# Kernel optimization log

Hardware: AMD Instinct MI355X
Metric: run time of the kernel (lower is better)

Reference implementation:

```python
import jax, jax.numpy as jnp
import numpy as np

COUPLING = 1.0
DT = 1.0
ATTR = 1.0
AFF_SCALE = 0.25          # feedback_affinity_scale
ALPHA_FAC = 0.25 * 1.0    # feedback_alpha_scale * alpha_scale (eval mode)
CHUNK = 256               # coupling_chunk_size
C_IN = 3                  # input_channels


def _pairwise_coupling(theta, spikes):
    """All-pairs vector Kuramoto coupling within one channel group.
    theta: [B, n, D], spikes: [B, n] -> [B, n, D]
    Chunked over receiver nodes i (lax.scan) to avoid [B,n,n,D] materialization."""
    B, n, D = theta.shape
    rng = jnp.clip(spikes.max(axis=1, keepdims=True) - spikes.min(axis=1, keepdims=True), 1e-6)  # [B,1]
    nchunks = n // CHUNK
    theta_i = theta.reshape(B, nchunks, CHUNK, D).transpose(1, 0, 2, 3)   # [nc,B,C,D]
    spike_i = spikes.reshape(B, nchunks, CHUNK).transpose(1, 0, 2)        # [nc,B,C]

    def body(_, xs):
        ti, si = xs                                              # [B,C,D], [B,C]
        nd = jnp.abs(si[:, :, None] - spikes[:, None, :]) / rng[:, :, None]   # [B,C,n]
        aff = AFF_SCALE * (1.0 - nd)
        alpha = ALPHA_FAC * nd
        # sin(theta_j - theta_i - alpha_ij): [B,C,n,D]
        phase = jnp.sin(theta[:, None, :, :] - ti[:, :, None, :] - alpha[..., None])
        out = (COUPLING / n) * jnp.sum(aff[..., None] * phase, axis=2)        # [B,C,D]
        return None, out

    _, outs = jax.lax.scan(body, None, (theta_i, spike_i))       # [nc,B,C,D]
    return outs.transpose(1, 0, 2, 3).reshape(B, n, D)


def _channel_wise_coupling(theta, spikes):
    """HWC flatten: channel c occupies nodes c, c+C, c+2C, ..."""
    B, N, D = theta.shape
    nc = N // C_IN
    th = theta.reshape(B, nc, C_IN, D).transpose(2, 0, 1, 3)     # [C_IN,B,nc,D]
    sp = spikes.reshape(B, nc, C_IN).transpose(2, 0, 1)          # [C_IN,B,nc]
    outs = jax.vmap(_pairwise_coupling)(th, sp)                  # [C_IN,B,nc,D]
    return outs.transpose(1, 2, 0, 3).reshape(B, N, D)


def setup_inputs() -> dict:
    key = jax.random.key(0)
    k1, k2, k3 = jax.random.split(key, 3)
    B, N, D = 4, 12288, 4
    return {
        "theta_prev": jax.random.normal(k1, (B, N, D), dtype=jnp.float32),
        "gamma_prev": jax.random.normal(k2, (B, N, D), dtype=jnp.float32),
        "affinity": jax.random.uniform(k3, (B, N), dtype=jnp.float32),
    }


def reference(theta_prev, gamma_prev, affinity):
    coupling_term = _channel_wise_coupling(theta_prev, affinity)
    theta_dot = ATTR * (gamma_prev - theta_prev) + coupling_term
    theta_next = theta_prev + DT * theta_dot
    # torch.nn.functional.normalize: x / max(||x||_2, eps)
    norm = jnp.maximum(jnp.linalg.norm(theta_next, axis=-1, keepdims=True), 1e-6)
    return theta_next / norm
```

## Files before the change

kernel.cpp:

```cpp
#include <hip/hip_runtime.h>
#include <math.h>

#define BATCH 4
#define NN    12288
#define CIN   3
#define NC    4096
#define NG    12
#define NB    128
#define HS3   3
#define PSZ   (4 * NB * 2)
#define HSTR  9

#define SC_OFF 0
#define P_OFF  64
#define H2_OFF (P_OFF + 192 * PSZ)

__launch_bounds__(256)
__global__ void k_hist(const float* __restrict__ spikes,
                       const float* __restrict__ theta,
                       float* __restrict__ ws) {
    __shared__ float lh[4 * NB * HS3];
    __shared__ float smn[4], smx[4];
    __shared__ float uScale, uAmin;

    int blk = blockIdx.x, g = blk >> 4, chunk = blk & 15;
    int b = g / CIN, c = g % CIN;
    int tid = threadIdx.x, lane = tid & 63, w = tid >> 6;

    #pragma unroll
    for (int q = 0; q < 6; ++q) lh[tid + q * 256] = 0.f;

    const float4* row = (const float4*)(spikes + b * NN);
    float mn = 1e30f, mx = -1e30f;
    #pragma unroll
    for (int q = 0; q < 12; ++q) {
        int f = tid + q * 256;
        float4 v4 = row[f];
        float e[4] = {v4.x, v4.y, v4.z, v4.w};
        int r  = (4 * f) % 3;
        int j0 = (c - r + 3) % 3;
        mn = fminf(mn, e[j0]); mx = fmaxf(mx, e[j0]);
        if (j0 + 3 < 4) { mn = fminf(mn, e[j0 + 3]); mx = fmaxf(mx, e[j0 + 3]); }
    }
    #pragma unroll
    for (int off = 32; off; off >>= 1) {
        mn = fminf(mn, __shfl_down(mn, off));
        mx = fmaxf(mx, __shfl_down(mx, off));
    }
    if (lane == 0) { smn[w] = mn; smx[w] = mx; }
    __syncthreads();
    if (tid == 0) {
        float m0 = fminf(fminf(smn[0], smn[1]), fminf(smn[2], smn[3]));
        float m1 = fmaxf(fmaxf(smx[0], smx[1]), fmaxf(smx[2], smx[3]));
        float scale = 0.25f / fmaxf(m1 - m0, 1e-6f);
        uScale = scale;
        uAmin  = m0 * scale;
    }
    __syncthreads();
    float scale = uScale, amin = uAmin;

    int k = chunk * 256 + tid;
    int v = b * NN + k * CIN + c;
    float a = spikes[v] * scale;
    int bb = (int)((a - amin) * (4.0f * NB));
    bb = bb < 0 ? 0 : (bb > NB - 1 ? NB - 1 : bb);
    float4 th = ((const float4*)theta)[v];
    float thv[4] = {th.x, th.y, th.z, th.w};
    #pragma unroll
    for (int d = 0; d < 4; ++d) {
        float sth, cth; __sincosf(thv[d], &sth, &cth);
        float* h = lh + (d * NB + bb) * HS3;
        atomicAdd(h + 0, sth);
        atomicAdd(h + 1, cth);
    }
    __syncthreads();

    float* P = ws + P_OFF + (size_t)blk * PSZ;
    #pragma unroll
    for (int q = 0; q < 4; ++q) {
        int o = tid + q * 256;
        P[o] = lh[(o >> 1) * HS3 + (o & 1)];
    }
    if (chunk == 0 && tid == 0) {
        ws[SC_OFF + g * 2]     = scale;
        ws[SC_OFF + g * 2 + 1] = amin;
    }
}

__launch_bounds__(256)
__global__ void k_mscan(float* __restrict__ ws) {
    __shared__ float raw[256];
    __shared__ float lh[NB * HSTR];
    int gd = blockIdx.x, g = gd >> 2, d = gd & 3;
    int tid = threadIdx.x, lane = tid & 63, w = tid >> 6;

    const float* Pg = ws + P_OFF + (size_t)(g * 16) * PSZ + d * (NB * 2);
    float s = 0.f;
    #pragma unroll
    for (int p = 0; p < 16; ++p) s += Pg[(size_t)p * PSZ + tid];
    raw[tid] = s;
    __syncthreads();

    float amin = ws[SC_OFF + g * 2 + 1];
    if (tid < NB) {
        float Ss = raw[tid * 2], Sc = raw[tid * 2 + 1];
        float abar = amin + ((float)tid + 0.5f) * (0.25f / (float)NB);
        float sa, ca; __sincosf(abar, &sa, &ca);
        float c0 = fmaf(ca, Ss,  sa * Sc);
        float c1 = fmaf(ca, Sc, -sa * Ss);
        float c4 = fmaf(ca, Ss, -sa * Sc);
        float c5 = fmaf(ca, Sc,  sa * Ss);
        float* L = lh + tid * HSTR;
        L[0] = c0;        L[1] = c1;
        L[2] = abar * c0; L[3] = abar * c1;
        L[4] = c4;        L[5] = c5;
        L[6] = abar * c4; L[7] = abar * c5;
    }
    __syncthreads();

    #pragma unroll
    for (int p = 0; p < 2; ++p) {
        int ch = w * 2 + p;
        float x0 = lh[(lane * 2 + 0) * HSTR + ch];
        float x1 = lh[(lane * 2 + 1) * HSTR + ch];
        float i0 = x0, i1 = i0 + x1;
        float incl = i1;
        #pragma unroll
        for (int off = 1; off < 64; off <<= 1) {
            float o = __shfl_up(incl, off);
            if (lane >= off) incl += o;
        }
        float ebt = incl - i1;
        lh[(lane * 2 + 0) * HSTR + ch] = ebt + i0;
        lh[(lane * 2 + 1) * HSTR + ch] = ebt + i1;
    }
    __syncthreads();

    float* H2 = ws + H2_OFF + (size_t)gd * (NB * 8);
    #pragma unroll
    for (int q = 0; q < 4; ++q) {
        int o = tid + q * 256;
        H2[o] = lh[(o >> 3) * HSTR + (o & 7)];
    }
}

__launch_bounds__(256)
__global__ void k_apply(const float* __restrict__ spikes,
                        const float* __restrict__ theta,
                        const float* __restrict__ gamma,
                        const float* __restrict__ ws,
                        float* __restrict__ out) {
    __shared__ __align__(16) float lH[CIN * 4 * NB * 8];
    int v = blockIdx.x * 256 + threadIdx.x;
    int b = v / NN;

    const float4* src = (const float4*)(ws + H2_OFF + (size_t)b * (CIN * 4 * NB * 8));
    float4* dst = (float4*)lH;
    #pragma unroll
    for (int q = 0; q < 12; ++q) {
        int i = threadIdx.x + q * 256;
        dst[i] = src[i];
    }
    __syncthreads();

    int r = v - b * NN;
    int c = r % 3;
    int g = b * CIN + c;
    float scale = ws[SC_OFF + g * 2], amin = ws[SC_OFF + g * 2 + 1];
    float a = spikes[v] * scale;
    int bb = (int)((a - amin) * (4.0f * NB));
    bb = bb < 0 ? 0 : (bb > NB - 1 ? NB - 1 : bb);
    float sa, ca; __sincosf(a, &sa, &ca);
    float4 th = ((const float4*)theta)[v];
    float4 gm = ((const float4*)gamma)[v];
    float thv[4] = {th.x, th.y, th.z, th.w};
    float cp[4];
    #pragma unroll
    for (int d = 0; d < 4; ++d) {
        float sth, cth; __sincosf(thv[d], &sth, &cth);
        float sf = fmaf(cth, sa,  sth * ca);
        float cf = fmaf(-sth, sa, cth * ca);
        float sp = fmaf(-cth, sa, sth * ca);
        float cq = fmaf(sth, sa,  cth * ca);
        const float4* Hq = (const float4*)(lH + (c * 4 + d) * (NB * 8));
        float4 Plo = Hq[bb * 2];
        float4 Phi = Hq[bb * 2 + 1];
        float4 T   = Hq[(NB - 1) * 2 + 1];
        float lowS = fmaf(0.25f - a, Plo.x, Plo.z);
        float lowC = fmaf(0.25f - a, Plo.y, Plo.w);
        float lower = cf * lowS - sf * lowC;
        float S4 = T.x - Phi.x, S5 = T.y - Phi.y;
        float S6 = T.z - Phi.z, S7 = T.w - Phi.w;
        float upS = fmaf(0.25f + a, S4, -S6);
        float upC = fmaf(0.25f + a, S5, -S7);
        float upper = cq * upS - sp * upC;
        cp[d] = (lower + upper) * (1.0f / (float)NC);
    }
    float tx = gm.x + cp[0], ty = gm.y + cp[1];
    float tz = gm.z + cp[2], tw = gm.w + cp[3];
    float nrm = sqrtf(tx * tx + ty * ty + tz * tz + tw * tw);
    float inv = 1.0f / fmaxf(nrm, 1e-6f);
    ((float4*)out)[v] = make_float4(tx * inv, ty * inv, tz * inv, tw * inv);
}

extern "C" void kernel_launch(void* const* d_in, const int* in_sizes, int n_in,
                              void* d_out, int out_size, void* d_ws, size_t ws_size,
                              hipStream_t stream) {
    const float* theta  = (const float*)d_in[0];
    const float* gamma  = (const float*)d_in[1];
    const float* spikes = (const float*)d_in[2];
    float* out = (float*)d_out;
    float* ws  = (float*)d_ws;

    hipLaunchKernelGGL(k_hist,  dim3(NG * 16),       dim3(256), 0, stream, spikes, theta, ws);
    hipLaunchKernelGGL(k_mscan, dim3(NG * 4),        dim3(256), 0, stream, ws);
    hipLaunchKernelGGL(k_apply, dim3(BATCH*NN/256),  dim3(256), 0, stream,
                       spikes, theta, gamma, ws, out);
}
```

Measured before the change: 70.89 us.

## Split stats into own kernel and parallelize hist/apply per dimension element

Moves the per-group min/max reduction into a separate k_stats kernel so k_hist no longer recomputes it in every block. k_hist now launches four times as many blocks, each thread handling one (node, dim) pair, and k_mscan reduces 64 partials instead of 16. k_apply maps one thread per output element, reads the prefix tables directly from global memory instead of staging them in LDS, and computes the norm with lane shuffles. This trades one extra launch, more partial-sum traffic and uncached table reads for more parallelism and no per-block LDS staging.

Result: slower. 75.31 us (+6.2%).

```diff
diff --git a/kernel.cpp b/kernel.cpp
--- a/kernel.cpp
+++ b/kernel.cpp
@@ -7,30 +7,17 @@
 #define NC    4096
 #define NG    12
 #define NB    128
-#define HS3   3
-#define PSZ   (4 * NB * 2)
 #define HSTR  9
 
 #define SC_OFF 0
 #define P_OFF  64
-#define H2_OFF (P_OFF + 192 * PSZ)
+#define H2_OFF (P_OFF + 768 * 1024)
 
 __launch_bounds__(256)
-__global__ void k_hist(const float* __restrict__ spikes,
-                       const float* __restrict__ theta,
-                       float* __restrict__ ws) {
-    __shared__ float lh[4 * NB * HS3];
-    __shared__ float smn[4], smx[4];
-    __shared__ float uScale, uAmin;
-
-    int blk = blockIdx.x, g = blk >> 4, chunk = blk & 15;
-    int b = g / CIN, c = g % CIN;
+__global__ void k_stats(const float* __restrict__ spikes, float* __restrict__ ws) {
+    int g = blockIdx.x, b = g / CIN, c = g % CIN;
+    const float4* row = (const float4*)(spikes + b * NN);
     int tid = threadIdx.x, lane = tid & 63, w = tid >> 6;
-
-    #pragma unroll
-    for (int q = 0; q < 6; ++q) lh[tid + q * 256] = 0.f;
-
-    const float4* row = (const float4*)(spikes + b * NN);
     float mn = 1e30f, mx = -1e30f;
     #pragma unroll
     for (int q = 0; q < 12; ++q) {
@@ -47,43 +34,48 @@
         mn = fminf(mn, __shfl_down(mn, off));
         mx = fmaxf(mx, __shfl_down(mx, off));
     }
+    __shared__ float smn[4], smx[4];
     if (lane == 0) { smn[w] = mn; smx[w] = mx; }
     __syncthreads();
     if (tid == 0) {
         float m0 = fminf(fminf(smn[0], smn[1]), fminf(smn[2], smn[3]));
         float m1 = fmaxf(fmaxf(smx[0], smx[1]), fmaxf(smx[2], smx[3]));
         float scale = 0.25f / fmaxf(m1 - m0, 1e-6f);
-        uScale = scale;
-        uAmin  = m0 * scale;
+        ws[SC_OFF + g * 2]     = scale;
+        ws[SC_OFF + g * 2 + 1] = m0 * scale;
     }
+}
+
+__launch_bounds__(256)
+__global__ void k_hist(const float* __restrict__ spikes,
+                       const float* __restrict__ theta,
+                       float* __restrict__ ws) {
+    __shared__ float lh[4 * NB * 3];
+    int blk = blockIdx.x, g = blk >> 6, j = blk & 63;
+    int b = g / CIN, c = g % CIN;
+    int tid = threadIdx.x;
+    #pragma unroll
+    for (int q = 0; q < 6; ++q) lh[tid + q * 256] = 0.f;
+    float scale = ws[SC_OFF + g * 2], amin = ws[SC_OFF + g * 2 + 1];
     __syncthreads();
-    float scale = uScale, amin = uAmin;
 
-    int k = chunk * 256 + tid;
+    int k = j * 64 + (tid >> 2);
+    int d = tid & 3;
     int v = b * NN + k * CIN + c;
     float a = spikes[v] * scale;
     int bb = (int)((a - amin) * (4.0f * NB));
     bb = bb < 0 ? 0 : (bb > NB - 1 ? NB - 1 : bb);
-    float4 th = ((const float4*)theta)[v];
-    float thv[4] = {th.x, th.y, th.z, th.w};
-    #pragma unroll
-    for (int d = 0; d < 4; ++d) {
-        float sth, cth; __sincosf(thv[d], &sth, &cth);
-        float* h = lh + (d * NB + bb) * HS3;
-        atomicAdd(h + 0, sth);
-        atomicAdd(h + 1, cth);
-    }
+    float sth, cth; __sincosf(theta[v * 4 + d], &sth, &cth);
+    float* h = lh + (d * NB + bb) * 3;
+    atomicAdd(h + 0, sth);
+    atomicAdd(h + 1, cth);
     __syncthreads();
 
-    float* P = ws + P_OFF + (size_t)blk * PSZ;
+    float* P = ws + P_OFF + (size_t)blk * 1024;
     #pragma unroll
     for (int q = 0; q < 4; ++q) {
         int o = tid + q * 256;
-        P[o] = lh[(o >> 1) * HS3 + (o & 1)];
-    }
-    if (chunk == 0 && tid == 0) {
-        ws[SC_OFF + g * 2]     = scale;
-        ws[SC_OFF + g * 2 + 1] = amin;
+        P[o] = lh[(o >> 1) * 3 + (o & 1)];
     }
 }
 
@@ -94,10 +86,10 @@
     int gd = blockIdx.x, g = gd >> 2, d = gd & 3;
     int tid = threadIdx.x, lane = tid & 63, w = tid >> 6;
 
-    const float* Pg = ws + P_OFF + (size_t)(g * 16) * PSZ + d * (NB * 2);
+    const float* Pg = ws + P_OFF + (size_t)(g * 64) * 1024 + d * 256;
     float s = 0.f;
-    #pragma unroll
-    for (int p = 0; p < 16; ++p) s += Pg[(size_t)p * PSZ + tid];
+    #pragma unroll 8
+    for (int p = 0; p < 64; ++p) s += Pg[(size_t)p * 1024 + tid];
     raw[tid] = s;
     __syncthreads();
 
@@ -150,57 +142,40 @@
                         const float* __restrict__ gamma,
                         const float* __restrict__ ws,
                         float* __restrict__ out) {
-    __shared__ __align__(16) float lH[CIN * 4 * NB * 8];
-    int v = blockIdx.x * 256 + threadIdx.x;
-    int b = v / NN;
-
-    const float4* src = (const float4*)(ws + H2_OFF + (size_t)b * (CIN * 4 * NB * 8));
-    float4* dst = (float4*)lH;
-    #pragma unroll
-    for (int q = 0; q < 12; ++q) {
-        int i = threadIdx.x + q * 256;
-        dst[i] = src[i];
-    }
-    __syncthreads();
-
-    int r = v - b * NN;
-    int c = r % 3;
+    int u = blockIdx.x * 256 + threadIdx.x;
+    int v = u >> 2, d = u & 3;
+    int b = u / (NN * 4);
+    int c = v % 3;
     int g = b * CIN + c;
     float scale = ws[SC_OFF + g * 2], amin = ws[SC_OFF + g * 2 + 1];
     float a = spikes[v] * scale;
     int bb = (int)((a - amin) * (4.0f * NB));
     bb = bb < 0 ? 0 : (bb > NB - 1 ? NB - 1 : bb);
     float sa, ca; __sincosf(a, &sa, &ca);
-    float4 th = ((const float4*)theta)[v];
-    float4 gm = ((const float4*)gamma)[v];
-    float thv[4] = {th.x, th.y, th.z, th.w};
-    float cp[4];
-    #pragma unroll
-    for (int d = 0; d < 4; ++d) {
-        float sth, cth; __sincosf(thv[d], &sth, &cth);
-        float sf = fmaf(cth, sa,  sth * ca);
-        float cf = fmaf(-sth, sa, cth * ca);
-        float sp = fmaf(-cth, sa, sth * ca);
-        float cq = fmaf(sth, sa,  cth * ca);
-        const float4* Hq = (const float4*)(lH + (c * 4 + d) * (NB * 8));
-        float4 Plo = Hq[bb * 2];
-        float4 Phi = Hq[bb * 2 + 1];
-        float4 T   = Hq[(NB - 1) * 2 + 1];
-        float lowS = fmaf(0.25f - a, Plo.x, Plo.z);
-        float lowC = fmaf(0.25f - a, Plo.y, Plo.w);
-        float lower = cf * lowS - sf * lowC;
-        float S4 = T.x - Phi.x, S5 = T.y - Phi.y;
-        float S6 = T.z - Phi.z, S7 = T.w - Phi.w;
-        float upS = fmaf(0.25f + a, S4, -S6);
-        float upC = fmaf(0.25f + a, S5, -S7);
-        float upper = cq * upS - sp * upC;
-        cp[d] = (lower + upper) * (1.0f / (float)NC);
-    }
-    float tx = gm.x + cp[0], ty = gm.y + cp[1];
-    float tz = gm.z + cp[2], tw = gm.w + cp[3];
-    float nrm = sqrtf(tx * tx + ty * ty + tz * tz + tw * tw);
-    float inv = 1.0f / fmaxf(nrm, 1e-6f);
-    ((float4*)out)[v] = make_float4(tx * inv, ty * inv, tz * inv, tw * inv);
+    float sth, cth; __sincosf(theta[u], &sth, &cth);
+    float sf = fmaf(cth, sa,  sth * ca);
+    float cf = fmaf(-sth, sa, cth * ca);
+    float sp = fmaf(-cth, sa, sth * ca);
+    float cq = fmaf(sth, sa,  cth * ca);
+    const float4* Hq = (const float4*)(ws + H2_OFF + (size_t)(g * 4 + d) * (NB * 8));
+    float4 Plo = Hq[bb * 2];
+    float4 Phi = Hq[bb * 2 + 1];
+    float4 T   = Hq[(NB - 1) * 2 + 1];
+    float lowS = fmaf(0.25f - a, Plo.x, Plo.z);
+    float lowC = fmaf(0.25f - a, Plo.y, Plo.w);
+    float lower = cf * lowS - sf * lowC;
+    float S4 = T.x - Phi.x, S5 = T.y - Phi.y;
+    float S6 = T.z - Phi.z, S7 = T.w - Phi.w;
+    float upS = fmaf(0.25f + a, S4, -S6);
+    float upC = fmaf(0.25f + a, S5, -S7);
+    float upper = cq * upS - sp * upC;
+    float cp = (lower + upper) * (1.0f / (float)NC);
+    float t = gamma[u] + cp;
+    float n2 = t * t;
+    n2 += __shfl_xor(n2, 1);
+    n2 += __shfl_xor(n2, 2);
+    float inv = 1.0f / fmaxf(sqrtf(n2), 1e-6f);
+    out[u] = t * inv;
 }
 
 extern "C" void kernel_launch(void* const* d_in, const int* in_sizes, int n_in,
@@ -212,8 +187,9 @@
     float* out = (float*)d_out;
     float* ws  = (float*)d_ws;
 
-    hipLaunchKernelGGL(k_hist,  dim3(NG * 16),       dim3(256), 0, stream, spikes, theta, ws);
-    hipLaunchKernelGGL(k_mscan, dim3(NG * 4),        dim3(256), 0, stream, ws);
-    hipLaunchKernelGGL(k_apply, dim3(BATCH*NN/256),  dim3(256), 0, stream,
+    hipLaunchKernelGGL(k_stats, dim3(NG),              dim3(256), 0, stream, spikes, ws);
+    hipLaunchKernelGGL(k_hist,  dim3(NG * 64),         dim3(256), 0, stream, spikes, theta, ws);
+    hipLaunchKernelGGL(k_mscan, dim3(NG * 4),          dim3(256), 0, stream, ws);
+    hipLaunchKernelGGL(k_apply, dim3(BATCH*NN*4/256),  dim3(256), 0, stream,
                        spikes, theta, gamma, ws, out);
 }
```

## Split min/max stats into separate kernel and coalesce histogram loads across channels

Applied to the files above, without the earlier changes.

Moves the per-group min/max reduction out of the histogram kernel into a small k_stats kernel, so the row is no longer re-reduced by every histogram block. The histogram kernel now handles contiguous nodes for all three channels with coalesced theta/spike loads, using a larger shared histogram indexed by channel. The merge-scan kernel sums 48 partials per batch instead of 16. In exchange there is an extra kernel launch and more partial-histogram traffic.

After: 72.93 us. 2.9% more time.

```diff
diff --git a/kernel.cpp b/kernel.cpp
--- a/kernel.cpp
+++ b/kernel.cpp
@@ -7,30 +7,19 @@
 #define NC    4096
 #define NG    12
 #define NB    128
-#define HS3   3
-#define PSZ   (4 * NB * 2)
 #define HSTR  9
+#define CPB   48
+#define PSZ   (CIN * 4 * NB * 2)
 
 #define SC_OFF 0
 #define P_OFF  64
-#define H2_OFF (P_OFF + 192 * PSZ)
-
-__launch_bounds__(256)
-__global__ void k_hist(const float* __restrict__ spikes,
-                       const float* __restrict__ theta,
-                       float* __restrict__ ws) {
-    __shared__ float lh[4 * NB * HS3];
-    __shared__ float smn[4], smx[4];
-    __shared__ float uScale, uAmin;
-
-    int blk = blockIdx.x, g = blk >> 4, chunk = blk & 15;
-    int b = g / CIN, c = g % CIN;
+#define H2_OFF (P_OFF + BATCH * CPB * PSZ)
+
+__launch_bounds__(256)
+__global__ void k_stats(const float* __restrict__ spikes, float* __restrict__ ws) {
+    int g = blockIdx.x, b = g / CIN, c = g % CIN;
+    const float4* row = (const float4*)(spikes + b * NN);
     int tid = threadIdx.x, lane = tid & 63, w = tid >> 6;
-
-    #pragma unroll
-    for (int q = 0; q < 6; ++q) lh[tid + q * 256] = 0.f;
-
-    const float4* row = (const float4*)(spikes + b * NN);
     float mn = 1e30f, mx = -1e30f;
     #pragma unroll
     for (int q = 0; q < 12; ++q) {
@@ -47,29 +36,44 @@
         mn = fminf(mn, __shfl_down(mn, off));
         mx = fmaxf(mx, __shfl_down(mx, off));
     }
+    __shared__ float smn[4], smx[4];
     if (lane == 0) { smn[w] = mn; smx[w] = mx; }
     __syncthreads();
     if (tid == 0) {
         float m0 = fminf(fminf(smn[0], smn[1]), fminf(smn[2], smn[3]));
         float m1 = fmaxf(fmaxf(smx[0], smx[1]), fmaxf(smx[2], smx[3]));
         float scale = 0.25f / fmaxf(m1 - m0, 1e-6f);
-        uScale = scale;
-        uAmin  = m0 * scale;
-    }
-    __syncthreads();
-    float scale = uScale, amin = uAmin;
-
-    int k = chunk * 256 + tid;
-    int v = b * NN + k * CIN + c;
+        ws[SC_OFF + g * 2]     = scale;
+        ws[SC_OFF + g * 2 + 1] = m0 * scale;
+    }
+}
+
+__launch_bounds__(256)
+__global__ void k_hist(const float* __restrict__ spikes,
+                       const float* __restrict__ theta,
+                       float* __restrict__ ws) {
+    __shared__ float lh[CIN * 4 * NB * 3];
+    int blk = blockIdx.x, b = blk / CPB, chunk = blk % CPB;
+    int tid = threadIdx.x;
+    #pragma unroll
+    for (int q = 0; q < 18; ++q) lh[tid + q * 256] = 0.f;
+
+    int r = chunk * 256 + tid;
+    int v = b * NN + r;
+    int c = r % 3;
+    float scale = ws[SC_OFF + (b * CIN + c) * 2];
+    float amin  = ws[SC_OFF + (b * CIN + c) * 2 + 1];
     float a = spikes[v] * scale;
     int bb = (int)((a - amin) * (4.0f * NB));
     bb = bb < 0 ? 0 : (bb > NB - 1 ? NB - 1 : bb);
     float4 th = ((const float4*)theta)[v];
     float thv[4] = {th.x, th.y, th.z, th.w};
+    __syncthreads();
+
     #pragma unroll
     for (int d = 0; d < 4; ++d) {
         float sth, cth; __sincosf(thv[d], &sth, &cth);
-        float* h = lh + (d * NB + bb) * HS3;
+        float* h = lh + ((c * 4 + d) * NB + bb) * 3;
         atomicAdd(h + 0, sth);
         atomicAdd(h + 1, cth);
     }
@@ -77,13 +81,9 @@
 
     float* P = ws + P_OFF + (size_t)blk * PSZ;
     #pragma unroll
-    for (int q = 0; q < 4; ++q) {
+    for (int q = 0; q < 12; ++q) {
         int o = tid + q * 256;
-        P[o] = lh[(o >> 1) * HS3 + (o & 1)];
-    }
-    if (chunk == 0 && tid == 0) {
-        ws[SC_OFF + g * 2]     = scale;
-        ws[SC_OFF + g * 2 + 1] = amin;
+        P[o] = lh[(o >> 1) * 3 + (o & 1)];
     }
 }
 
@@ -92,12 +92,13 @@
     __shared__ float raw[256];
     __shared__ float lh[NB * HSTR];
     int gd = blockIdx.x, g = gd >> 2, d = gd & 3;
+    int b = g / CIN, c = g % CIN;
     int tid = threadIdx.x, lane = tid & 63, w = tid >> 6;
 
-    const float* Pg = ws + P_OFF + (size_t)(g * 16) * PSZ + d * (NB * 2);
+    const float* Pg = ws + P_OFF + (size_t)(b * CPB) * PSZ + (c * 4 + d) * (NB * 2);
     float s = 0.f;
-    #pragma unroll
-    for (int p = 0; p < 16; ++p) s += Pg[(size_t)p * PSZ + tid];
+    #pragma unroll 8
+    for (int p = 0; p < CPB; ++p) s += Pg[(size_t)p * PSZ + tid];
     raw[tid] = s;
     __syncthreads();
 
@@ -212,8 +213,9 @@
     float* out = (float*)d_out;
     float* ws  = (float*)d_ws;
 
-    hipLaunchKernelGGL(k_hist,  dim3(NG * 16),       dim3(256), 0, stream, spikes, theta, ws);
-    hipLaunchKernelGGL(k_mscan, dim3(NG * 4),        dim3(256), 0, stream, ws);
-    hipLaunchKernelGGL(k_apply, dim3(BATCH*NN/256),  dim3(256), 0, stream,
+    hipLaunchKernelGGL(k_stats, dim3(NG),             dim3(256), 0, stream, spikes, ws);
+    hipLaunchKernelGGL(k_hist,  dim3(BATCH * CPB),    dim3(256), 0, stream, spikes, theta, ws);
+    hipLaunchKernelGGL(k_mscan, dim3(NG * 4),         dim3(256), 0, stream, ws);
+    hipLaunchKernelGGL(k_apply, dim3(BATCH*NN/256),   dim3(256), 0, stream,
                        spikes, theta, gamma, ws, out);
 }
```
